# Kernel optimization log

Hardware: AMD Instinct MI355X
Metric: run time of the kernel (lower is better)

## Reference

```python
import jax, jax.numpy as jnp
import numpy as np


def _closest_dist_sum(p1, p2):
    # p1: [B, N, 3], p2: [B, M, 3]
    # Euclidean distance via the expanded quadratic form; matches
    # torch.norm(p1 - p2, 2, dim=3) -> min over p2 -> sum over all.
    d2 = (jnp.sum(p1 * p1, axis=-1)[:, :, None]
          + jnp.sum(p2 * p2, axis=-1)[:, None, :]
          - 2.0 * jnp.einsum('bnd,bmd->bnm', p1, p2))  # [B, N, M]
    d = jnp.sqrt(jnp.maximum(d2, 0.0))
    return jnp.sum(jnp.min(d, axis=2))


def setup_inputs() -> dict:
    key = jax.random.key(0)
    k1, k2 = jax.random.split(key)
    shape_xyz = jax.random.normal(k1, (8, 8192, 6), dtype=jnp.float32)
    skel_xyz = jax.random.normal(k2, (8, 2048, 3), dtype=jnp.float32)
    return {"shape_xyz": shape_xyz, "skel_xyz": skel_xyz}


def reference(shape_xyz, skel_xyz):
    # normals (shape_xyz[:, :, 3:6]) are extracted but unused in the loss
    pts = shape_xyz[:, :, :3]
    cd1 = _closest_dist_sum(pts, skel_xyz)   # shape -> skeleton
    cd2 = _closest_dist_sum(skel_xyz, pts)   # skeleton -> shape
    loss_cd = (cd1 + cd2) * 0.0001
    return loss_cd
```

## Files before the change

### kernel.cpp

```cpp
#include <hip/hip_runtime.h>

#define BATCH   8
#define SHAPE_N 8192
#define SKEL_M  2048

template <int SA, int SB, int NA, int NB>
__device__ __forceinline__ void cd_dir(
    const float* __restrict__ A, const float* __restrict__ B,
    unsigned int* __restrict__ ws, int b, int a0, int c0, int tid,
    float4* sB)
{
    {
        const float* q = B + ((size_t)b * NB + c0 + tid) * SB;
        const float qx = q[0], qy = q[1], qz = q[2];
        sB[tid] = make_float4(-2.f * qx, -2.f * qy, -2.f * qz,
                              qx * qx + qy * qy + qz * qz);
    }

    const float* Ab = A + (size_t)b * NA * SA;
    float ax[4], ay[4], az[4], ra[4], dmin[4];
#pragma unroll
    for (int k = 0; k < 4; ++k) {
        const float* p = Ab + (size_t)(a0 + k * 256 + tid) * SA;
        ax[k] = p[0]; ay[k] = p[1]; az[k] = p[2];
        ra[k] = ax[k] * ax[k] + ay[k] * ay[k] + az[k] * az[k];
        dmin[k] = 3.4e38f;
    }
    __syncthreads();

#pragma unroll 8
    for (int i = 0; i < 256; ++i) {
        float4 q = sB[i];
#pragma unroll
        for (int k = 0; k < 4; ++k) {
            float t = ra[k] + q.w;
            t = fmaf(ax[k], q.x, t);
            t = fmaf(ay[k], q.y, t);
            t = fmaf(az[k], q.z, t);
            dmin[k] = fminf(dmin[k], t);
        }
    }

    unsigned int* wsb = ws + (size_t)b * NA;
#pragma unroll
    for (int k = 0; k < 4; ++k)
        atomicMin(&wsb[a0 + k * 256 + tid],
                  __float_as_uint(fmaxf(dmin[k], 0.f)));
}

__global__ __launch_bounds__(256) void cd_main(
    const float* __restrict__ shape, const float* __restrict__ skel,
    unsigned int* __restrict__ ws, float* __restrict__ out)
{
    __shared__ float4 sB[256];
    const int tid = threadIdx.x;
    const int bid = blockIdx.x;
    if (bid == 0 && tid == 0) out[0] = 0.f;
    if (bid < 512) {
        const int b = bid >> 6, rem = bid & 63;
        cd_dir<6, 3, SHAPE_N, SKEL_M>(shape, skel, ws,
                                      b, (rem >> 3) * 1024, (rem & 7) * 256, tid, sB);
    } else {
        const int j = bid - 512;
        const int b = j >> 6, rem = j & 63;
        cd_dir<3, 6, SKEL_M, SHAPE_N>(skel, shape, ws + (size_t)BATCH * SHAPE_N,
                                      b, (rem >> 5) * 1024, (rem & 31) * 256, tid, sB);
    }
}

__global__ __launch_bounds__(256) void cd_finalize(
    const uint4* __restrict__ ws, float* __restrict__ out)
{
    __shared__ float s_wsum[4];
    const uint4 v = ws[blockIdx.x * 256 + threadIdx.x];
    float s = sqrtf(__uint_as_float(v.x)) + sqrtf(__uint_as_float(v.y)) +
              sqrtf(__uint_as_float(v.z)) + sqrtf(__uint_as_float(v.w));
    for (int off = 32; off; off >>= 1) s += __shfl_down(s, off, 64);
    const int lane = threadIdx.x & 63, wave = threadIdx.x >> 6;
    if (lane == 0) s_wsum[wave] = s;
    __syncthreads();
    if (threadIdx.x == 0) {
        atomicAdd(out, (s_wsum[0] + s_wsum[1] + s_wsum[2] + s_wsum[3]) * 1e-4f);
    }
}

extern "C" void kernel_launch(void* const* d_in, const int* in_sizes, int n_in,
                              void* d_out, int out_size, void* d_ws, size_t ws_size,
                              hipStream_t stream) {
    const float* shape = (const float*)d_in[0];
    const float* skel  = (const float*)d_in[1];
    float* out         = (float*)d_out;
    unsigned int* ws   = (unsigned int*)d_ws;

    hipMemsetAsync(ws, 0xFF,
                   (size_t)BATCH * (SHAPE_N + SKEL_M) * sizeof(unsigned int),
                   stream);
    cd_main<<<1024, 256, 0, stream>>>(shape, skel, ws, out);
    cd_finalize<<<BATCH * (SHAPE_N + SKEL_M) / 1024, 256, 0, stream>>>(
        (const uint4*)ws, out);
}
```

Baseline: 84.35 us.

## Replace atomicMin reduction with per-chunk partial minima and larger per-thread tiles

Each thread now holds 8 query points instead of 4, so every shared-memory load is reused across more FMAs, and the block count is halved to 512. Each block writes its partial minima to a workspace slice instead of doing atomicMin, and the finalize kernel takes the min across chunks before the sqrt-sum. The per-point norm term is added once after the loop rather than inside it. This removes the workspace memset and the atomics, at the cost of more workspace traffic, more registers per thread, fewer blocks to fill the GPU, and a heavier finalize kernel.

```diff
diff --git a/kernel.cpp b/kernel.cpp
--- a/kernel.cpp
+++ b/kernel.cpp
@@ -4,84 +4,97 @@
 #define SHAPE_N 8192
 #define SKEL_M  2048
 
-template <int SA, int SB, int NA, int NB>
+#define WS2_OFF (BATCH * 4 * 8 * 2048)
+
+template <int SA, int SB, int NA, int NB, int NG, int NC>
 __device__ __forceinline__ void cd_dir(
     const float* __restrict__ A, const float* __restrict__ B,
-    unsigned int* __restrict__ ws, int b, int a0, int c0, int tid,
-    float4* sB)
+    float* __restrict__ ws, int b, int g, int c, int tid, float4* sB)
 {
     {
-        const float* q = B + ((size_t)b * NB + c0 + tid) * SB;
+        const float* q = B + ((size_t)b * NB + c * 256 + tid) * SB;
         const float qx = q[0], qy = q[1], qz = q[2];
         sB[tid] = make_float4(-2.f * qx, -2.f * qy, -2.f * qz,
                               qx * qx + qy * qy + qz * qz);
     }
 
-    const float* Ab = A + (size_t)b * NA * SA;
-    float ax[4], ay[4], az[4], ra[4], dmin[4];
+    const float* Ab = A + ((size_t)b * NA + g * 2048) * SA;
+    float ax[8], ay[8], az[8], ra[8], dmin[8];
 #pragma unroll
-    for (int k = 0; k < 4; ++k) {
-        const float* p = Ab + (size_t)(a0 + k * 256 + tid) * SA;
+    for (int k = 0; k < 8; ++k) {
+        const float* p = Ab + (size_t)(k * 256 + tid) * SA;
         ax[k] = p[0]; ay[k] = p[1]; az[k] = p[2];
         ra[k] = ax[k] * ax[k] + ay[k] * ay[k] + az[k] * az[k];
         dmin[k] = 3.4e38f;
     }
     __syncthreads();
 
-#pragma unroll 8
+#pragma unroll 4
     for (int i = 0; i < 256; ++i) {
         float4 q = sB[i];
 #pragma unroll
-        for (int k = 0; k < 4; ++k) {
-            float t = ra[k] + q.w;
-            t = fmaf(ax[k], q.x, t);
+        for (int k = 0; k < 8; ++k) {
+            float t = fmaf(ax[k], q.x, q.w);
             t = fmaf(ay[k], q.y, t);
             t = fmaf(az[k], q.z, t);
             dmin[k] = fminf(dmin[k], t);
         }
     }
 
-    unsigned int* wsb = ws + (size_t)b * NA;
+    float* w = ws + ((size_t)(b * NG + g) * NC + c) * 2048;
 #pragma unroll
-    for (int k = 0; k < 4; ++k)
-        atomicMin(&wsb[a0 + k * 256 + tid],
-                  __float_as_uint(fmaxf(dmin[k], 0.f)));
+    for (int k = 0; k < 8; ++k)
+        w[k * 256 + tid] = dmin[k] + ra[k];
 }
 
 __global__ __launch_bounds__(256) void cd_main(
     const float* __restrict__ shape, const float* __restrict__ skel,
-    unsigned int* __restrict__ ws, float* __restrict__ out)
+    float* __restrict__ ws)
 {
     __shared__ float4 sB[256];
     const int tid = threadIdx.x;
     const int bid = blockIdx.x;
-    if (bid == 0 && tid == 0) out[0] = 0.f;
-    if (bid < 512) {
-        const int b = bid >> 6, rem = bid & 63;
-        cd_dir<6, 3, SHAPE_N, SKEL_M>(shape, skel, ws,
-                                      b, (rem >> 3) * 1024, (rem & 7) * 256, tid, sB);
+    if (bid < 256) {
+        cd_dir<6, 3, SHAPE_N, SKEL_M, 4, 8>(
+            shape, skel, ws, bid >> 5, (bid >> 3) & 3, bid & 7, tid, sB);
     } else {
-        const int j = bid - 512;
-        const int b = j >> 6, rem = j & 63;
-        cd_dir<3, 6, SKEL_M, SHAPE_N>(skel, shape, ws + (size_t)BATCH * SHAPE_N,
-                                      b, (rem >> 5) * 1024, (rem & 31) * 256, tid, sB);
+        const int j = bid - 256;
+        cd_dir<3, 6, SKEL_M, SHAPE_N, 1, 32>(
+            skel, shape, ws + WS2_OFF, j >> 5, 0, j & 31, tid, sB);
     }
 }
 
 __global__ __launch_bounds__(256) void cd_finalize(
-    const uint4* __restrict__ ws, float* __restrict__ out)
+    const float* __restrict__ ws, float* __restrict__ out)
 {
     __shared__ float s_wsum[4];
-    const uint4 v = ws[blockIdx.x * 256 + threadIdx.x];
-    float s = sqrtf(__uint_as_float(v.x)) + sqrtf(__uint_as_float(v.y)) +
-              sqrtf(__uint_as_float(v.z)) + sqrtf(__uint_as_float(v.w));
+    const int tid = threadIdx.x;
+    const int bid = blockIdx.x;
+    float m;
+    if (bid < 256) {
+        const int p = bid * 256 + tid;
+        const int bg = p >> 11;
+        const int idx = p & 2047;
+        const float* w = ws + ((size_t)bg * 8) * 2048 + idx;
+        m = w[0];
+#pragma unroll
+        for (int c = 1; c < 8; ++c) m = fminf(m, w[c * 2048]);
+    } else {
+        const int p = (bid - 256) * 256 + tid;
+        const int b = p >> 11;
+        const int idx = p & 2047;
+        const float* w = ws + WS2_OFF + ((size_t)b * 32) * 2048 + idx;
+        m = w[0];
+#pragma unroll
+        for (int c = 1; c < 32; ++c) m = fminf(m, w[c * 2048]);
+    }
+    float s = sqrtf(fmaxf(m, 0.f));
     for (int off = 32; off; off >>= 1) s += __shfl_down(s, off, 64);
-    const int lane = threadIdx.x & 63, wave = threadIdx.x >> 6;
+    const int lane = tid & 63, wave = tid >> 6;
     if (lane == 0) s_wsum[wave] = s;
     __syncthreads();
-    if (threadIdx.x == 0) {
+    if (tid == 0)
         atomicAdd(out, (s_wsum[0] + s_wsum[1] + s_wsum[2] + s_wsum[3]) * 1e-4f);
-    }
 }
 
 extern "C" void kernel_launch(void* const* d_in, const int* in_sizes, int n_in,
@@ -90,12 +103,9 @@
     const float* shape = (const float*)d_in[0];
     const float* skel  = (const float*)d_in[1];
     float* out         = (float*)d_out;
-    unsigned int* ws   = (unsigned int*)d_ws;
+    float* ws          = (float*)d_ws;
 
-    hipMemsetAsync(ws, 0xFF,
-                   (size_t)BATCH * (SHAPE_N + SKEL_M) * sizeof(unsigned int),
-                   stream);
-    cd_main<<<1024, 256, 0, stream>>>(shape, skel, ws, out);
-    cd_finalize<<<BATCH * (SHAPE_N + SKEL_M) / 1024, 256, 0, stream>>>(
-        (const uint4*)ws, out);
+    hipMemsetAsync(out, 0, sizeof(float), stream);
+    cd_main<<<512, 256, 0, stream>>>(shape, skel, ws);
+    cd_finalize<<<320, 256, 0, stream>>>(ws, out);
 }
```

New measurement: 85.44 us. About the same (+1.3%).
